# Kernel optimization log

Hardware: AMD Instinct MI355X
Metric: run time of the kernel (lower is better)

## Reference

```python
import jax, jax.numpy as jnp
import numpy as np

EPS = 1e-5
TCOUNT = 18  # SBNet tiles per spatial dim -> 10x10 px tiles on 180x180 map
NUM_HEADS = 6
NUM_ATTRS = 5


def _conv(x, w, groups=1):
    # 3x3 stride-1 'SAME' conv, NCHW / OIHW
    return jax.lax.conv_general_dilated(
        x, w, window_strides=(1, 1), padding='SAME',
        dimension_numbers=('NCHW', 'OIHW', 'NCHW'),
        feature_group_count=groups)


def _bn(y, g, b, m, v):
    scale = g / jnp.sqrt(v + EPS)
    return y * scale[None, :, None, None] + (b - m * scale)[None, :, None, None]


def _mask_px(tile_mask, H, W):
    # expand [B, ty, tx] tile activity to per-pixel mask [B, 1, H, W]
    ty, tx = tile_mask.shape[1], tile_mask.shape[2]
    m = tile_mask.astype(jnp.float32)
    m = jnp.repeat(jnp.repeat(m, H // ty, axis=1), W // tx, axis=2)
    return m[:, None]


def setup_inputs() -> dict:
    key = jax.random.key(0)
    ks = jax.random.split(key, 24)
    B, C, H, W = 2, 512, 180, 180
    SC = 64                       # SHARED_CONV_CHANNEL
    HM1 = SC * NUM_HEADS          # 384
    HM2 = 2 * NUM_HEADS           # hm_max_ch * num_heads = 12
    AT1 = SC * NUM_HEADS * NUM_ATTRS  # 1920
    AT2 = 3 * NUM_ATTRS * NUM_HEADS   # attr_max_ch * 5 * 6 = 90

    def w(k, o, i):
        return jax.random.normal(k, (o, i, 3, 3), jnp.float32) * (1.0 / np.sqrt(i * 9))

    inp = {
        'x': jax.random.normal(ks[0], (B, C, H, W), jnp.float32),
        'tile_mask': jax.random.randint(ks[1], (B, TCOUNT, TCOUNT), 0, 2, jnp.int32),
        'w_shared': w(ks[2], SC, C),
        'g_s': jax.random.uniform(ks[3], (SC,), jnp.float32, 0.5, 1.5),
        'b_s': jax.random.normal(ks[4], (SC,)) * 0.1,
        'm_s': jax.random.normal(ks[5], (SC,)) * 0.1,
        'v_s': jax.random.uniform(ks[6], (SC,), jnp.float32, 0.5, 1.5),
        'w_hm1': w(ks[7], HM1, SC),
        'g_h': jax.random.uniform(ks[8], (HM1,), jnp.float32, 0.5, 1.5),
        'b_h': jax.random.normal(ks[9], (HM1,)) * 0.1,
        'm_h': jax.random.normal(ks[10], (HM1,)) * 0.1,
        'v_h': jax.random.uniform(ks[11], (HM1,), jnp.float32, 0.5, 1.5),
        'w_hm2': w(ks[12], HM2, SC),  # groups=6 -> in_per_group = 384/6 = 64
        'bias_hm': jnp.full((HM2,), -2.19, jnp.float32),  # fill_bias(-2.19)
        'w_attr1': w(ks[13], AT1, SC),
        'g_a': jax.random.uniform(ks[14], (AT1,), jnp.float32, 0.5, 1.5),
        'b_a': jax.random.normal(ks[15], (AT1,)) * 0.1,
        'm_a': jax.random.normal(ks[16], (AT1,)) * 0.1,
        'v_a': jax.random.uniform(ks[17], (AT1,), jnp.float32, 0.5, 1.5),
        'w_attr2': w(ks[18], AT2, SC),  # groups=30 -> in_per_group = 1920/30 = 64
        'bias_attr': jnp.zeros((AT2,), jnp.float32),
    }
    return inp


def reference(x, tile_mask, w_shared, g_s, b_s, m_s, v_s,
              w_hm1, g_h, b_h, m_h, v_h, w_hm2, bias_hm,
              w_attr1, g_a, b_a, m_a, v_a, w_attr2, bias_attr):
    B, _, H, W = x.shape
    mp = _mask_px(tile_mask, H, W)  # SBNet active-tile scatter mask

    # shared conv: gather active tiles -> conv -> BN -> ReLU -> scatter
    xg = x * mp
    shared = jax.nn.relu(_bn(_conv(xg, w_shared), g_s, b_s, m_s, v_s)) * mp

    # heatmap branch: Conv-BN-ReLU (64 -> 384, groups=1) then grouped conv (groups=6)
    h = jax.nn.relu(_bn(_conv(shared, w_hm1), g_h, b_h, m_h, v_h)) * mp
    hm = (_conv(h, w_hm2, groups=NUM_HEADS) + bias_hm[None, :, None, None]) * mp

    # attribute branch: Conv-BN-ReLU (64 -> 1920, groups=1) then grouped conv (groups=30)
    a = jax.nn.relu(_bn(_conv(shared, w_attr1), g_a, b_a, m_a, v_a)) * mp
    attr = (_conv(a, w_attr2, groups=NUM_HEADS * NUM_ATTRS)
            + bias_attr[None, :, None, None]) * mp

    # per-head slices are static index ranges of these tensors (heatmap_outp_inds /
    # attr_outp_inds); return the full stacked maps concatenated on channels.
    return jnp.concatenate([hm, attr], axis=1)  # [B, 12+90, H, W]
```

## Files before the change

kernel.cpp:

```cpp
#include <hip/hip_runtime.h>
#include <cstdint>

#define TC 18
#define HW 180
#define EPSF 1e-5f

typedef _Float16 half8 __attribute__((ext_vector_type(8)));
typedef _Float16 half4 __attribute__((ext_vector_type(4)));
typedef float f32x4 __attribute__((ext_vector_type(4)));

#define OFF_SHB  0
#define N_SHB    (2*HW*HW*64)
#define OFF_WSH  (N_SHB)
#define N_WSH    (9*64*512)
#define OFF_WM   (OFF_WSH + N_WSH)
#define N_WM     (36*9*64*64)
#define OFF_W2   (OFF_WM + N_WM)
#define N_W2     (36*9*16*64)

__global__ __launch_bounds__(256) void prep_kernel(
    const float* __restrict__ w_s, const float* __restrict__ w_hm1,
    const float* __restrict__ w_attr1, const float* __restrict__ w_hm2,
    const float* __restrict__ w_attr2, _Float16* __restrict__ ws) {
  int i = blockIdx.x * 256 + threadIdx.x;
  if (i < N_WSH) {
    int ic = i & 511, oc = (i >> 9) & 63, tap = i >> 15;
    ws[OFF_WSH + i] = (_Float16)w_s[((size_t)(oc*512 + ic))*9 + tap];
    return;
  }
  i -= N_WSH;
  if (i < N_WM) {
    int ic = i & 63, oc = (i >> 6) & 63, tap = (i >> 12) % 9, g = i / 36864;
    float v;
    if (g < 6) v = w_hm1[((size_t)((g*64 + oc)*64 + ic))*9 + tap];
    else       v = w_attr1[((size_t)(((g-6)*64 + oc)*64 + ic))*9 + tap];
    ws[OFF_WM + i] = (_Float16)v;
    return;
  }
  i -= N_WM;
  if (i < N_W2) {
    int ic = i & 63, oc = (i >> 6) & 15, tap = (i >> 10) % 9, g = i / 9216;
    float v = 0.f;
    if (g < 6) { if (oc < 2) v = w_hm2[((size_t)((g*2 + oc)*64 + ic))*9 + tap]; }
    else       { if (oc < 3) v = w_attr2[((size_t)(((g-6)*3 + oc)*64 + ic))*9 + tap]; }
    ws[OFF_W2 + i] = (_Float16)v;
  }
}

__global__ __launch_bounds__(256, 4) void shared_conv_mfma(
    const float* __restrict__ x, const int* __restrict__ tmask,
    const _Float16* __restrict__ wsh,
    const float* __restrict__ g_s, const float* __restrict__ b_s,
    const float* __restrict__ m_s, const float* __restrict__ v_s,
    _Float16* __restrict__ shb) {
  int bid = blockIdx.x;
  int b = bid / (TC*TC), t = bid % (TC*TC);
  int ty = t / TC, tx = t % TC;
  int Y0 = ty*10, X0 = tx*10;
  int tid = threadIdx.x;
  _Float16* shp = shb + (size_t)b*HW*HW*64;
  bool active = tmask[b*TC*TC + t] != 0;
  if (!active) {
    for (int i = tid; i < 1600; i += 256) {
      int px = i >> 4, q = i & 15;
      int gy = Y0 + px/10, gx = X0 + px%10;
      *(float2*)(shp + ((size_t)(gy*HW + gx))*64 + q*4) = make_float2(0.f, 0.f);
    }
    return;
  }
  int nact = 0;
  #pragma unroll
  for (int dy = 0; dy < 3; dy++)
    #pragma unroll
    for (int dx = 0; dx < 3; dx++) {
      int tyy = ty+dy-1, txx = tx+dx-1;
      int a = (tyy>=0 && tyy<TC && txx>=0 && txx<TC) ? tmask[b*TC*TC + tyy*TC + txx] : 0;
      nact |= (a != 0) << (dy*3+dx);
    }
  __shared__ _Float16 sm[144*64];
  int lane = tid & 63, w = tid >> 6;
  int mh = w >> 1, nh = w & 1;
  int l15 = lane & 15, l4 = lane >> 4;
  int r0[4];
  #pragma unroll
  for (int fi = 0; fi < 4; fi++) {
    int f = mh + fi*2;
    int p = f*16 + l15; if (p > 99) p = 99;
    r0[fi] = (p/10)*12 + (p%10);
  }
  f32x4 acc[4][2];
  #pragma unroll
  for (int fi = 0; fi < 4; fi++)
    #pragma unroll
    for (int j = 0; j < 2; j++) acc[fi][j] = (f32x4)0.f;

  for (int ck = 0; ck < 8; ck++) {
    __syncthreads();
    for (int i = tid; i < 1152; i += 256) {
      int px = i % 144, s8 = i / 144;
      int ry = px/12, rx = px%12;
      int gy = Y0-1+ry, gx = X0-1+rx;
      int selr = (ry==0)?0:((ry<=10)?1:2);
      int selc = (rx==0)?0:((rx<=10)?1:2);
      bool ok = (gy>=0 && gy<HW && gx>=0 && gx<HW) && ((nact>>(selr*3+selc))&1);
      half8 hv;
      #pragma unroll
      for (int j = 0; j < 8; j++) hv[j] = (_Float16)0.f;
      if (ok) {
        const float* xp = x + (((size_t)b*512 + ck*64 + s8*8)*HW + gy)*HW + gx;
        #pragma unroll
        for (int j = 0; j < 8; j++) hv[j] = (_Float16)xp[(size_t)j*HW*HW];
      }
      *(half8*)((char*)sm + px*128 + (((s8 ^ (px&7)) & 7)<<4)) = hv;
    }
    __syncthreads();
    for (int tap = 0; tap < 9; tap++) {
      int ky = tap/3, kx = tap%3;
      int radd = ky*12 + kx;
      #pragma unroll
      for (int ks = 0; ks < 2; ks++) {
        half8 bf[2];
        #pragma unroll
        for (int j = 0; j < 2; j++) {
          int oc = (nh*2 + j)*16 + l15;
          bf[j] = *(const half8*)(wsh + (size_t)(tap*64 + oc)*512 + ck*64 + ks*32 + l4*8);
        }
        #pragma unroll
        for (int fi = 0; fi < 4; fi++) {
          int f = mh + fi*2;
          if (f < 7) {
            int r = r0[fi] + radd;
            half8 af = *(const half8*)((const char*)sm + (r<<7) + ((((ks*4 + l4) ^ r) & 7)<<4));
            acc[fi][0] = __builtin_amdgcn_mfma_f32_16x16x32_f16(bf[0], af, acc[fi][0], 0, 0, 0);
            acc[fi][1] = __builtin_amdgcn_mfma_f32_16x16x32_f16(bf[1], af, acc[fi][1], 0, 0, 0);
          }
        }
      }
    }
  }
  float sc4[2][4], sh4[2][4];
  #pragma unroll
  for (int j = 0; j < 2; j++) {
    int ocb = (nh*2 + j)*16 + l4*4;
    float4 gg = *(const float4*)&g_s[ocb];
    float4 vv = *(const float4*)&v_s[ocb];
    float4 bb = *(const float4*)&b_s[ocb];
    float4 mm = *(const float4*)&m_s[ocb];
    float gA[4] = {gg.x,gg.y,gg.z,gg.w}, vA[4] = {vv.x,vv.y,vv.z,vv.w};
    float bA[4] = {bb.x,bb.y,bb.z,bb.w}, mA[4] = {mm.x,mm.y,mm.z,mm.w};
    #pragma unroll
    for (int r = 0; r < 4; r++) {
      float s = gA[r] * rsqrtf(vA[r] + EPSF);
      sc4[j][r] = s; sh4[j][r] = bA[r] - mA[r]*s;
    }
  }
  #pragma unroll
  for (int fi = 0; fi < 4; fi++) {
    int f = mh + fi*2;
    if (f < 7) {
      int p = f*16 + l15;
      if (p < 100) {
        int gy = Y0 + p/10, gx = X0 + p%10;
        _Float16* dst = shp + ((size_t)(gy*HW + gx))*64;
        #pragma unroll
        for (int j = 0; j < 2; j++) {
          int ocb = (nh*2 + j)*16 + l4*4;
          half4 hv;
          #pragma unroll
          for (int r = 0; r < 4; r++)
            hv[r] = (_Float16)fmaxf(fmaf(acc[fi][j][r], sc4[j][r], sh4[j][r]), 0.f);
          *(half4*)(dst + ocb) = hv;
        }
      }
    }
  }
}

__global__ __launch_bounds__(256, 3) void branch_conv_mfma(
    const _Float16* __restrict__ shb, const int* __restrict__ tmask,
    const _Float16* __restrict__ wm, const _Float16* __restrict__ w2,
    const float* __restrict__ g_h, const float* __restrict__ b_h,
    const float* __restrict__ m_h, const float* __restrict__ v_h,
    const float* __restrict__ g_a, const float* __restrict__ b_a,
    const float* __restrict__ m_a, const float* __restrict__ v_a,
    const float* __restrict__ bias_hm, const float* __restrict__ bias_attr,
    float* __restrict__ out) {
  int bid = blockIdx.x;
  int g2 = bid % 18;
  int t = bid / 18;
  int b = t / (TC*TC); t %= (TC*TC);
  int ty = t / TC, tx = t % TC;
  int Y0 = ty*10, X0 = tx*10;
  int tid = threadIdx.x;
  bool active = tmask[b*TC*TC + ty*TC + tx] != 0;
  if (!active) {
    if (tid < 100) {
      int py = tid/10, pxx = tid%10;
      #pragma unroll
      for (int gi = 0; gi < 2; gi++) {
        int g = g2*2 + gi;
        int Oc = (g < 6) ? 2 : 3;
        int cobase = (g < 6) ? g*2 : 12 + (g-6)*3;
        for (int o = 0; o < Oc; o++)
          out[(((size_t)b*102 + cobase + o)*HW + (Y0+py))*HW + (X0+pxx)] = 0.f;
      }
    }
    return;
  }
  int nact = 0;
  #pragma unroll
  for (int dy = 0; dy < 3; dy++)
    #pragma unroll
    for (int dx = 0; dx < 3; dx++) {
      int tyy = ty+dy-1, txx = tx+dx-1;
      int a = (tyy>=0 && tyy<TC && txx>=0 && txx<TC) ? tmask[b*TC*TC + tyy*TC + txx] : 0;
      nact |= (a != 0) << (dy*3+dx);
    }
  __shared__ _Float16 sm[(196 + 144)*64];
  const _Float16* shp = shb + (size_t)b*HW*HW*64;
  int lane = tid & 63, w = tid >> 6;
  int gi = w & 1, m = w >> 1;
  int g = g2*2 + gi;
  int l15 = lane & 15, l4 = lane >> 4;

  for (int i = tid; i < 1568; i += 256) {
    int px = i >> 3, s8 = i & 7;
    int ry = px/14, rx = px%14;
    int gy = Y0-2+ry, gx = X0-2+rx;
    half8 hv;
    if (gy>=0 && gy<HW && gx>=0 && gx<HW)
      hv = *(const half8*)(shp + ((size_t)(gy*HW + gx))*64 + s8*8);
    else {
      #pragma unroll
      for (int j = 0; j < 8; j++) hv[j] = (_Float16)0.f;
    }
    *(half8*)((char*)sm + px*128 + (((s8 ^ px) & 7)<<4)) = hv;
  }
  __syncthreads();

  int r0[5];
  #pragma unroll
  for (int fi = 0; fi < 5; fi++) {
    int gf = m*5 + fi;
    int p = gf*16 + l15; if (p > 143) p = 143;
    r0[fi] = (p/12)*14 + (p%12);
  }
  f32x4 acc[5][4];
  #pragma unroll
  for (int fi = 0; fi < 5; fi++)
    #pragma unroll
    for (int nf = 0; nf < 4; nf++) acc[fi][nf] = (f32x4)0.f;

  const _Float16* wmg = wm + (size_t)g*9*64*64;
  for (int tap = 0; tap < 9; tap++) {
    int radd = (tap/3)*14 + (tap%3);
    #pragma unroll
    for (int ks = 0; ks < 2; ks++) {
      half8 bf[4];
      #pragma unroll
      for (int nf = 0; nf < 4; nf++)
        bf[nf] = *(const half8*)(wmg + (size_t)(tap*64 + nf*16 + l15)*64 + ks*32 + l4*8);
      #pragma unroll
      for (int fi = 0; fi < 5; fi++) {
        int gf = m*5 + fi;
        if (gf < 9) {
          int r = r0[fi] + radd;
          half8 af = *(const half8*)((const char*)sm + (r<<7) + ((((ks*4 + l4) ^ r) & 7)<<4));
          #pragma unroll
          for (int nf = 0; nf < 4; nf++)
            acc[fi][nf] = __builtin_amdgcn_mfma_f32_16x16x32_f16(bf[nf], af, acc[fi][nf], 0, 0, 0);
        }
      }
    }
  }

  {
    int cbase = (g < 6) ? g*64 : (g-6)*64;
    const float* GG = (g < 6) ? g_h : g_a;
    const float* VV = (g < 6) ? v_h : v_a;
    const float* BB = (g < 6) ? b_h : b_a;
    const float* MM = (g < 6) ? m_h : m_a;
    float sc4[4][4], sh4[4][4];
    #pragma unroll
    for (int nf = 0; nf < 4; nf++) {
      int c = cbase + nf*16 + l4*4;
      float4 gg = *(const float4*)&GG[c];
      float4 vv = *(const float4*)&VV[c];
      float4 bb = *(const float4*)&BB[c];
      float4 mm = *(const float4*)&MM[c];
      float gA[4] = {gg.x,gg.y,gg.z,gg.w}, vA[4] = {vv.x,vv.y,vv.z,vv.w};
      float bA[4] = {bb.x,bb.y,bb.z,bb.w}, mA[4] = {mm.x,mm.y,mm.z,mm.w};
      #pragma unroll
      for (int r = 0; r < 4; r++) {
        float s = gA[r] * rsqrtf(vA[r] + EPSF);
        sc4[nf][r] = s; sh4[nf][r] = bA[r] - mA[r]*s;
      }
    }
    #pragma unroll
    for (int phase = 0; phase < 2; phase++) {
      if (gi == phase) {
        _Float16* hb = (phase == 0) ? (_Float16*)sm + 196*64 : (_Float16*)sm;
        #pragma unroll
        for (int fi = 0; fi < 5; fi++) {
          int gf = m*5 + fi;
          if (gf < 9) {
            int px = gf*16 + l15;
            int hy = px/12, hx = px - hy*12;
            int selr = (hy==0)?0:((hy<=10)?1:2);
            int selc = (hx==0)?0:((hx<=10)?1:2);
            bool ok = (nact>>(selr*3+selc)) & 1;
            #pragma unroll
            for (int nf = 0; nf < 4; nf++) {
              int ocb = nf*16 + l4*4;
              half4 hv;
              #pragma unroll
              for (int r = 0; r < 4; r++) {
                float v = ok ? fmaxf(fmaf(acc[fi][nf][r], sc4[nf][r], sh4[nf][r]), 0.f) : 0.f;
                hv[r] = (_Float16)v;
              }
              *(half4*)((char*)hb + (px<<7) + ((((ocb>>3) ^ px) & 7)<<4) + (ocb&7)*2) = hv;
            }
          }
        }
      }
      __syncthreads();
    }
  }

  const _Float16* hb = (gi == 0) ? (const _Float16*)sm + 196*64 : (const _Float16*)sm;
  int r0b[4];
  #pragma unroll
  for (int fi = 0; fi < 4; fi++) {
    int f = m*4 + fi;
    int p = f*16 + l15; if (p > 99) p = 99;
    r0b[fi] = (p/10)*12 + (p%10);
  }
  f32x4 acc2[4];
  #pragma unroll
  for (int fi = 0; fi < 4; fi++) acc2[fi] = (f32x4)0.f;
  const _Float16* w2g = w2 + (size_t)g*9*16*64;
  for (int tap = 0; tap < 9; tap++) {
    int radd = (tap/3)*12 + (tap%3);
    #pragma unroll
    for (int ks = 0; ks < 2; ks++) {
      half8 bf = *(const half8*)(w2g + (size_t)(tap*16 + l15)*64 + ks*32 + l4*8);
      #pragma unroll
      for (int fi = 0; fi < 4; fi++) {
        int f = m*4 + fi;
        if (f < 7) {
          int r = r0b[fi] + radd;
          half8 af = *(const half8*)((const char*)hb + (r<<7) + ((((ks*4 + l4) ^ r) & 7)<<4));
          acc2[fi] = __builtin_amdgcn_mfma_f32_16x16x32_f16(bf, af, acc2[fi], 0, 0, 0);
        }
      }
    }
  }
  int Oc = (g < 6) ? 2 : 3;
  int cobase = (g < 6) ? g*2 : 12 + (g-6)*3;
  float bo[3];
  #pragma unroll
  for (int o = 0; o < 3; o++)
    bo[o] = (o < Oc) ? ((g < 6) ? bias_hm[g*2 + o] : bias_attr[(g-6)*3 + o]) : 0.f;
  #pragma unroll
  for (int fi = 0; fi < 4; fi++) {
    int f = m*4 + fi;
    int p = f*16 + l15;
    if (f < 7 && l4 == 0 && p < 100) {
      int gy = Y0 + p/10, gx = X0 + p%10;
      float* op = out + (((size_t)b*102 + cobase)*HW + gy)*HW + gx;
      #pragma unroll
      for (int o = 0; o < 3; o++)
        if (o < Oc) op[(size_t)o*HW*HW] = acc2[fi][o] + bo[o];
    }
  }
}

extern "C" void kernel_launch(void* const* d_in, const int* in_sizes, int n_in,
                              void* d_out, int out_size, void* d_ws, size_t ws_size,
                              hipStream_t stream) {
  const float* x        = (const float*)d_in[0];
  const int*   tmask    = (const int*)  d_in[1];
  const float* w_s      = (const float*)d_in[2];
  const float* g_s      = (const float*)d_in[3];
  const float* b_s      = (const float*)d_in[4];
  const float* m_s      = (const float*)d_in[5];
  const float* v_s      = (const float*)d_in[6];
  const float* w_hm1    = (const float*)d_in[7];
  const float* g_h      = (const float*)d_in[8];
  const float* b_h      = (const float*)d_in[9];
  const float* m_h      = (const float*)d_in[10];
  const float* v_h      = (const float*)d_in[11];
  const float* w_hm2    = (const float*)d_in[12];
  const float* bias_hm  = (const float*)d_in[13];
  const float* w_attr1  = (const float*)d_in[14];
  const float* g_a      = (const float*)d_in[15];
  const float* b_a      = (const float*)d_in[16];
  const float* m_a      = (const float*)d_in[17];
  const float* v_a      = (const float*)d_in[18];
  const float* w_attr2  = (const float*)d_in[19];
  const float* bias_attr= (const float*)d_in[20];
  _Float16* ws = (_Float16*)d_ws;
  float* out = (float*)d_out;

  int prep_total = N_WSH + N_WM + N_W2;
  prep_kernel<<<(prep_total + 255)/256, 256, 0, stream>>>(
      w_s, w_hm1, w_attr1, w_hm2, w_attr2, ws);
  shared_conv_mfma<<<2*TC*TC, 256, 0, stream>>>(
      x, tmask, ws + OFF_WSH, g_s, b_s, m_s, v_s, ws + OFF_SHB);
  branch_conv_mfma<<<2*TC*TC*18, 256, 0, stream>>>(
      ws + OFF_SHB, tmask, ws + OFF_WM, ws + OFF_W2,
      g_h, b_h, m_h, v_h, g_a, b_a, m_a, v_a, bias_hm, bias_attr, out);
}
```

Baseline: 655.4 us.

## Pre-transpose input to NHWC fp16 before shared conv

```diff
diff --git a/kernel.cpp b/kernel.cpp
--- a/kernel.cpp
+++ b/kernel.cpp
@@ -17,6 +17,8 @@
 #define N_WM     (36*9*64*64)
 #define OFF_W2   (OFF_WM + N_WM)
 #define N_W2     (36*9*16*64)
+#define OFF_XH   (OFF_W2 + N_W2)
+#define N_XH     ((size_t)2*HW*HW*512)
 
 __global__ __launch_bounds__(256) void prep_kernel(
     const float* __restrict__ w_s, const float* __restrict__ w_hm1,
@@ -47,7 +49,171 @@
   }
 }
 
-__global__ __launch_bounds__(256, 4) void shared_conv_mfma(
+__global__ __launch_bounds__(256) void transpose_nhwc(
+    const float* __restrict__ x, const int* __restrict__ tmask,
+    _Float16* __restrict__ xh) {
+  int bid = blockIdx.x;
+  int b = bid / (TC*TC), t = bid % (TC*TC);
+  int ty = t / TC, tx = t % TC;
+  int Y0 = ty*10, X0 = tx*10;
+  int tid = threadIdx.x;
+  _Float16* xp = xh + (size_t)b*HW*HW*512;
+  bool active = tmask[b*TC*TC + t] != 0;
+  if (!active) {
+    half8 z;
+    #pragma unroll
+    for (int j = 0; j < 8; j++) z[j] = (_Float16)0.f;
+    for (int i = tid; i < 6400; i += 256) {
+      int px = i >> 6, s = i & 63;
+      int gy = Y0 + px/10, gx = X0 + px%10;
+      *(half8*)(xp + ((size_t)(gy*HW + gx))*512 + s*8) = z;
+    }
+    return;
+  }
+  __shared__ float lds[64][101];
+  for (int ck = 0; ck < 8; ck++) {
+    __syncthreads();
+    for (int i = tid; i < 6400; i += 256) {
+      int c = i / 100, px = i % 100;
+      int gy = Y0 + px/10, gx = X0 + px%10;
+      lds[c][px] = x[(((size_t)b*512 + ck*64 + c)*HW + gy)*HW + gx];
+    }
+    __syncthreads();
+    for (int i = tid; i < 800; i += 256) {
+      int px = i >> 3, s = i & 7;
+      int gy = Y0 + px/10, gx = X0 + px%10;
+      half8 hv;
+      #pragma unroll
+      for (int k = 0; k < 8; k++) hv[k] = (_Float16)lds[s*8 + k][px];
+      *(half8*)(xp + ((size_t)(gy*HW + gx))*512 + ck*64 + s*8) = hv;
+    }
+  }
+}
+
+__device__ __forceinline__ void shared_epilogue(
+    f32x4 (&acc)[4][2], int mh, int nh, int l15, int l4, int Y0, int X0,
+    const float* g_s, const float* b_s, const float* m_s, const float* v_s,
+    _Float16* shp) {
+  float sc4[2][4], sh4[2][4];
+  #pragma unroll
+  for (int j = 0; j < 2; j++) {
+    int ocb = (nh*2 + j)*16 + l4*4;
+    float4 gg = *(const float4*)&g_s[ocb];
+    float4 vv = *(const float4*)&v_s[ocb];
+    float4 bb = *(const float4*)&b_s[ocb];
+    float4 mm = *(const float4*)&m_s[ocb];
+    float gA[4] = {gg.x,gg.y,gg.z,gg.w}, vA[4] = {vv.x,vv.y,vv.z,vv.w};
+    float bA[4] = {bb.x,bb.y,bb.z,bb.w}, mA[4] = {mm.x,mm.y,mm.z,mm.w};
+    #pragma unroll
+    for (int r = 0; r < 4; r++) {
+      float s = gA[r] * rsqrtf(vA[r] + EPSF);
+      sc4[j][r] = s; sh4[j][r] = bA[r] - mA[r]*s;
+    }
+  }
+  #pragma unroll
+  for (int fi = 0; fi < 4; fi++) {
+    int f = mh + fi*2;
+    if (f < 7) {
+      int p = f*16 + l15;
+      if (p < 100) {
+        int gy = Y0 + p/10, gx = X0 + p%10;
+        _Float16* dst = shp + ((size_t)(gy*HW + gx))*64;
+        #pragma unroll
+        for (int j = 0; j < 2; j++) {
+          int ocb = (nh*2 + j)*16 + l4*4;
+          half4 hv;
+          #pragma unroll
+          for (int r = 0; r < 4; r++)
+            hv[r] = (_Float16)fmaxf(fmaf(acc[fi][j][r], sc4[j][r], sh4[j][r]), 0.f);
+          *(half4*)(dst + ocb) = hv;
+        }
+      }
+    }
+  }
+}
+
+__global__ __launch_bounds__(256, 4) void shared_conv_mfma_xh(
+    const _Float16* __restrict__ xh, const int* __restrict__ tmask,
+    const _Float16* __restrict__ wsh,
+    const float* __restrict__ g_s, const float* __restrict__ b_s,
+    const float* __restrict__ m_s, const float* __restrict__ v_s,
+    _Float16* __restrict__ shb) {
+  int bid = blockIdx.x;
+  int b = bid / (TC*TC), t = bid % (TC*TC);
+  int ty = t / TC, tx = t % TC;
+  int Y0 = ty*10, X0 = tx*10;
+  int tid = threadIdx.x;
+  _Float16* shp = shb + (size_t)b*HW*HW*64;
+  bool active = tmask[b*TC*TC + t] != 0;
+  if (!active) {
+    for (int i = tid; i < 1600; i += 256) {
+      int px = i >> 4, q = i & 15;
+      int gy = Y0 + px/10, gx = X0 + px%10;
+      *(float2*)(shp + ((size_t)(gy*HW + gx))*64 + q*4) = make_float2(0.f, 0.f);
+    }
+    return;
+  }
+  const _Float16* xhp = xh + (size_t)b*HW*HW*512;
+  __shared__ _Float16 sm[144*64];
+  int lane = tid & 63, w = tid >> 6;
+  int mh = w >> 1, nh = w & 1;
+  int l15 = lane & 15, l4 = lane >> 4;
+  int r0[4];
+  #pragma unroll
+  for (int fi = 0; fi < 4; fi++) {
+    int f = mh + fi*2;
+    int p = f*16 + l15; if (p > 99) p = 99;
+    r0[fi] = (p/10)*12 + (p%10);
+  }
+  f32x4 acc[4][2];
+  #pragma unroll
+  for (int fi = 0; fi < 4; fi++)
+    #pragma unroll
+    for (int j = 0; j < 2; j++) acc[fi][j] = (f32x4)0.f;
+
+  for (int ck = 0; ck < 8; ck++) {
+    __syncthreads();
+    for (int i = tid; i < 1152; i += 256) {
+      int px = i >> 3, s8 = i & 7;
+      int ry = px/12, rx = px%12;
+      int gy = Y0-1+ry, gx = X0-1+rx;
+      half8 hv;
+      if (gy >= 0 && gy < HW && gx >= 0 && gx < HW)
+        hv = *(const half8*)(xhp + ((size_t)(gy*HW + gx))*512 + ck*64 + s8*8);
+      else {
+        #pragma unroll
+        for (int j = 0; j < 8; j++) hv[j] = (_Float16)0.f;
+      }
+      *(half8*)((char*)sm + px*128 + (((s8 ^ px) & 7)<<4)) = hv;
+    }
+    __syncthreads();
+    for (int tap = 0; tap < 9; tap++) {
+      int radd = (tap/3)*12 + (tap%3);
+      #pragma unroll
+      for (int ks = 0; ks < 2; ks++) {
+        half8 bf[2];
+        #pragma unroll
+        for (int j = 0; j < 2; j++) {
+          int oc = (nh*2 + j)*16 + l15;
+          bf[j] = *(const half8*)(wsh + (size_t)(tap*64 + oc)*512 + ck*64 + ks*32 + l4*8);
+        }
+        #pragma unroll
+        for (int fi = 0; fi < 4; fi++) {
+          int f = mh + fi*2;
+          if (f < 7) {
+            int r = r0[fi] + radd;
+            half8 af = *(const half8*)((const char*)sm + (r<<7) + ((((ks*4 + l4) ^ r) & 7)<<4));
+            acc[fi][0] = __builtin_amdgcn_mfma_f32_16x16x32_f16(bf[0], af, acc[fi][0], 0, 0, 0);
+            acc[fi][1] = __builtin_amdgcn_mfma_f32_16x16x32_f16(bf[1], af, acc[fi][1], 0, 0, 0);
+          }
+        }
+      }
+    }
+  }
+  shared_epilogue(acc, mh, nh, l15, l4, Y0, X0, g_s, b_s, m_s, v_s, shp);
+}
+
+__global__ __launch_bounds__(256, 4) void shared_conv_mfma_nchw(
     const float* __restrict__ x, const int* __restrict__ tmask,
     const _Float16* __restrict__ wsh,
     const float* __restrict__ g_s, const float* __restrict__ b_s,
@@ -115,8 +281,7 @@
     }
     __syncthreads();
     for (int tap = 0; tap < 9; tap++) {
-      int ky = tap/3, kx = tap%3;
-      int radd = ky*12 + kx;
+      int radd = (tap/3)*12 + (tap%3);
       #pragma unroll
       for (int ks = 0; ks < 2; ks++) {
         half8 bf[2];
@@ -138,42 +303,7 @@
       }
     }
   }
-  float sc4[2][4], sh4[2][4];
-  #pragma unroll
-  for (int j = 0; j < 2; j++) {
-    int ocb = (nh*2 + j)*16 + l4*4;
-    float4 gg = *(const float4*)&g_s[ocb];
-    float4 vv = *(const float4*)&v_s[ocb];
-    float4 bb = *(const float4*)&b_s[ocb];
-    float4 mm = *(const float4*)&m_s[ocb];
-    float gA[4] = {gg.x,gg.y,gg.z,gg.w}, vA[4] = {vv.x,vv.y,vv.z,vv.w};
-    float bA[4] = {bb.x,bb.y,bb.z,bb.w}, mA[4] = {mm.x,mm.y,mm.z,mm.w};
-    #pragma unroll
-    for (int r = 0; r < 4; r++) {
-      float s = gA[r] * rsqrtf(vA[r] + EPSF);
-      sc4[j][r] = s; sh4[j][r] = bA[r] - mA[r]*s;
-    }
-  }
-  #pragma unroll
-  for (int fi = 0; fi < 4; fi++) {
-    int f = mh + fi*2;
-    if (f < 7) {
-      int p = f*16 + l15;
-      if (p < 100) {
-        int gy = Y0 + p/10, gx = X0 + p%10;
-        _Float16* dst = shp + ((size_t)(gy*HW + gx))*64;
-        #pragma unroll
-        for (int j = 0; j < 2; j++) {
-          int ocb = (nh*2 + j)*16 + l4*4;
-          half4 hv;
-          #pragma unroll
-          for (int r = 0; r < 4; r++)
-            hv[r] = (_Float16)fmaxf(fmaf(acc[fi][j][r], sc4[j][r], sh4[j][r]), 0.f);
-          *(half4*)(dst + ocb) = hv;
-        }
-      }
-    }
-  }
+  shared_epilogue(acc, mh, nh, l15, l4, Y0, X0, g_s, b_s, m_s, v_s, shp);
 }
 
 __global__ __launch_bounds__(256, 3) void branch_conv_mfma(
@@ -405,8 +535,16 @@
   int prep_total = N_WSH + N_WM + N_W2;
   prep_kernel<<<(prep_total + 255)/256, 256, 0, stream>>>(
       w_s, w_hm1, w_attr1, w_hm2, w_attr2, ws);
-  shared_conv_mfma<<<2*TC*TC, 256, 0, stream>>>(
-      x, tmask, ws + OFF_WSH, g_s, b_s, m_s, v_s, ws + OFF_SHB);
+
+  size_t need_bytes = ((size_t)OFF_XH + N_XH) * sizeof(_Float16);
+  if (ws_size >= need_bytes) {
+    transpose_nhwc<<<2*TC*TC, 256, 0, stream>>>(x, tmask, ws + OFF_XH);
+    shared_conv_mfma_xh<<<2*TC*TC, 256, 0, stream>>>(
+        ws + OFF_XH, tmask, ws + OFF_WSH, g_s, b_s, m_s, v_s, ws + OFF_SHB);
+  } else {
+    shared_conv_mfma_nchw<<<2*TC*TC, 256, 0, stream>>>(
+        x, tmask, ws + OFF_WSH, g_s, b_s, m_s, v_s, ws + OFF_SHB);
+  }
   branch_conv_mfma<<<2*TC*TC*18, 256, 0, stream>>>(
       ws + OFF_SHB, tmask, ws + OFF_WM, ws + OFF_W2,
       g_h, b_h, m_h, v_h, g_a, b_a, m_a, v_a, bias_hm, bias_attr, out);
```

Measured after the change: 712.7 us. +8.7%, slower.
